# Kernel optimization log

Hardware: AMD Instinct MI355X
Metric: run time of the kernel (lower is better)

## Reference

```python
import math
import jax, jax.numpy as jnp
import numpy as np

B, N, C = 2, 2048, 256
TOPK_COARSE = 128
TOPK_FINE = 16
LOCAL_RAD = math.radians(15.0)
TEMP = 0.07
NEG = -1e9


def setup_inputs() -> dict:
    key = jax.random.key(0)
    ks = jax.random.split(key, 8)
    feat_a = jax.random.normal(ks[0], (B, N, C), jnp.float32)
    feat_b = jax.random.normal(ks[1], (B, N, C), jnp.float32)
    da = jax.random.normal(ks[2], (B, N, 3), jnp.float32)
    db = jax.random.normal(ks[3], (B, N, 3), jnp.float32)
    dirs_a = da / jnp.linalg.norm(da, axis=-1, keepdims=True)
    dirs_b = db / jnp.linalg.norm(db, axis=-1, keepdims=True)
    s = 1.0 / np.sqrt(C).astype(np.float32)
    Wq = jax.random.normal(ks[4], (C, C), jnp.float32) * s
    bq = jax.random.normal(ks[5], (C,), jnp.float32) * 0.01
    Wk = jax.random.normal(ks[6], (C, C), jnp.float32) * s
    bk = jax.random.normal(ks[7], (C,), jnp.float32) * 0.01
    return {"feat_a": feat_a, "feat_b": feat_b, "dirs_a": dirs_a, "dirs_b": dirs_b,
            "Wq": Wq, "bq": bq, "Wk": Wk, "bk": bk}


def reference(feat_a, feat_b, dirs_a, dirs_b, Wq, bq, Wk, bk):
    b, n, c = feat_a.shape
    q = feat_a @ Wq.T + bq                         # [B,N,C]
    k = feat_b @ Wk.T + bk                         # [B,N,C]

    # coarse stage: top-k over full similarity (math identical to chunked topk)
    sim = jnp.einsum('bnc,bmc->bnm', q, k)         # [B,N,N]
    _, coarse_idx = jax.lax.top_k(sim, TOPK_COARSE)  # [B,N,Kc]

    bi = jnp.arange(b)[:, None, None]
    k_cand = k[bi, coarse_idx]                     # [B,N,Kc,C]
    db_cand = dirs_b[bi, coarse_idx]               # [B,N,Kc,3]

    # angular locality mask (non-differentiable path)
    cosang = jnp.clip(jnp.sum(dirs_a[:, :, None, :] * db_cand, -1), -1.0, 1.0)
    ang = jnp.arccos(jax.lax.stop_gradient(cosang))
    local_mask = ang <= LOCAL_RAD                  # [B,N,Kc]
    # per-row fallback to all-ones (subsumes the chunk-level torch.any check)
    valid = local_mask.any(-1, keepdims=True)
    eff = jnp.where(valid, local_mask, True)

    logits_full = jnp.einsum('bnc,bnkc->bnk', q, k_cand) / TEMP
    logits_full = jnp.where(eff, logits_full, NEG)

    # fine stage: keep top TOPK_FINE candidates per row
    topk_vals, topk_pos = jax.lax.top_k(logits_full, TOPK_FINE)  # [B,N,Kf]
    idx = jnp.take_along_axis(coarse_idx, topk_pos, -1)
    eff_f = jnp.take_along_axis(eff, topk_pos, -1)
    fallback = eff_f.any(-1, keepdims=True)
    eff_f = jnp.where(fallback, eff_f, True)
    logits = jnp.where(eff_f, topk_vals, NEG)

    probs = jax.nn.softmax(logits, axis=-1) * eff_f.astype(logits.dtype)

    # scatter sparse support into dense P (indices distinct per row -> set is safe)
    ri = jnp.arange(n)[None, :, None]
    P = jnp.zeros((b, n, n), feat_a.dtype).at[bi, ri, idx].set(probs)
    P = P / (P.sum(-1, keepdims=True) + 1e-8)
    return P
```

## Files before the change

kernel.cpp:

```cpp
#include <hip/hip_runtime.h>
#include <hip/hip_bf16.h>
#include <math.h>

#define NN_ 2048
#define CC_ 256
#define KC_ 128
#define KF_ 16
#define EQCAP 64

typedef __attribute__((ext_vector_type(8))) short short8;
typedef __attribute__((ext_vector_type(4))) float f32x4;

__device__ __forceinline__ unsigned int mono_u(float f) {
  unsigned int u = __float_as_uint(f);
  return (u & 0x80000000u) ? ~u : (u | 0x80000000u);
}
__device__ __forceinline__ float inv_mono(unsigned int m) {
  unsigned int u = (m & 0x80000000u) ? (m ^ 0x80000000u) : ~m;
  return __uint_as_float(u);
}

__device__ __forceinline__ void gload_lds16(const void* g, void* l) {
  __builtin_amdgcn_global_load_lds(
      (const __attribute__((address_space(1))) void*)g,
      (__attribute__((address_space(3))) void*)l, 16, 0, 0);
}

__global__ __launch_bounds__(256) void proj_split_kernel(
    const float* __restrict__ fa, const float* __restrict__ fb,
    const float* __restrict__ Wq, const float* __restrict__ bq,
    const float* __restrict__ Wk, const float* __restrict__ bk,
    __hip_bfloat16* __restrict__ qh, __hip_bfloat16* __restrict__ ql,
    __hip_bfloat16* __restrict__ kh, __hip_bfloat16* __restrict__ kl)
{
  __shared__ float As2[32][32];
  __shared__ float Bs[32][64];
  const int z = blockIdx.z;
  const float* A = z ? fb : fa;
  const float* W = z ? Wk : Wq;
  const float* bias = z ? bk : bq;
  __hip_bfloat16* oh = z ? kh : qh;
  __hip_bfloat16* ol = z ? kl : ql;

  const int m0 = blockIdx.y * 32, n0 = blockIdx.x * 64;
  const int tid = threadIdx.x;
  const int tx = tid & 15, ty = tid >> 4;
  const int r = tid >> 3, c4 = (tid & 7) << 2;
  float acc[2][4] = {};
  for (int kb = 0; kb < CC_; kb += 32) {
    float4 va = *(const float4*)(A + (long)(m0 + r) * CC_ + kb + c4);
    As2[c4 + 0][r] = va.x; As2[c4 + 1][r] = va.y;
    As2[c4 + 2][r] = va.z; As2[c4 + 3][r] = va.w;
    float4 vb0 = *(const float4*)(W + (long)(n0 + r) * CC_ + kb + c4);
    Bs[c4 + 0][r] = vb0.x; Bs[c4 + 1][r] = vb0.y;
    Bs[c4 + 2][r] = vb0.z; Bs[c4 + 3][r] = vb0.w;
    float4 vb1 = *(const float4*)(W + (long)(n0 + r + 32) * CC_ + kb + c4);
    Bs[c4 + 0][r + 32] = vb1.x; Bs[c4 + 1][r + 32] = vb1.y;
    Bs[c4 + 2][r + 32] = vb1.z; Bs[c4 + 3][r + 32] = vb1.w;
    __syncthreads();
#pragma unroll
    for (int kk = 0; kk < 32; ++kk) {
      float a0 = As2[kk][(ty << 1)];
      float a1 = As2[kk][(ty << 1) + 1];
      float4 bv = *(const float4*)&Bs[kk][tx << 2];
      acc[0][0] += a0 * bv.x; acc[0][1] += a0 * bv.y;
      acc[0][2] += a0 * bv.z; acc[0][3] += a0 * bv.w;
      acc[1][0] += a1 * bv.x; acc[1][1] += a1 * bv.y;
      acc[1][2] += a1 * bv.z; acc[1][3] += a1 * bv.w;
    }
    __syncthreads();
  }
  float bv4[4];
#pragma unroll
  for (int j = 0; j < 4; ++j) bv4[j] = bias[n0 + (tx << 2) + j];
#pragma unroll
  for (int i = 0; i < 2; ++i) {
    int m = m0 + (ty << 1) + i;
    __hip_bfloat16 hv[4], lv[4];
#pragma unroll
    for (int j = 0; j < 4; ++j) {
      float v = acc[i][j] + bv4[j];
      __hip_bfloat16 h = __float2bfloat16(v);
      hv[j] = h;
      lv[j] = __float2bfloat16(v - __bfloat162float(h));
    }
    long base = (long)m * CC_ + n0 + (tx << 2);
    *(uint2*)(oh + base) = *(const uint2*)hv;
    *(uint2*)(ol + base) = *(const uint2*)lv;
  }
}

__global__ __launch_bounds__(256) void sim_mfma_kernel(
    const __hip_bfloat16* __restrict__ qh, const __hip_bfloat16* __restrict__ ql,
    const __hip_bfloat16* __restrict__ kh, const __hip_bfloat16* __restrict__ kl,
    float* __restrict__ sim)
{
  __shared__ short As[128 * 32];
  __shared__ short Bs[128 * 32];
  const int z = blockIdx.z;
  const long off = (long)z * NN_ * CC_;
  const __hip_bfloat16* Aseg[3] = {qh + off, qh + off, ql + off};
  const __hip_bfloat16* Bseg[3] = {kh + off, kl + off, kh + off};
  const int m0 = blockIdx.y * 128, n0 = blockIdx.x * 128;
  const int tid = threadIdx.x;
  const int lane = tid & 63, wave = tid >> 6;
  const int wm = (wave & 1) << 6, wn = (wave >> 1) << 6;
  const int fm = lane & 15, quad = lane >> 4;

  const int r0 = tid >> 2, r1 = r0 + 64;
  const int c0 = (((tid & 3) ^ ((r0 >> 1) & 3)) << 3);
  const int c1 = (((tid & 3) ^ ((r1 >> 1) & 3)) << 3);
  short* lA0 = As + (long)tid * 8;
  short* lA1 = As + ((long)tid + 256) * 8;
  short* lB0 = Bs + (long)tid * 8;
  short* lB1 = Bs + ((long)tid + 256) * 8;
  const long gA0 = (long)(m0 + r0) * CC_ + c0;
  const long gA1 = (long)(m0 + r1) * CC_ + c1;
  const long gB0 = (long)(n0 + r0) * CC_ + c0;
  const long gB1 = (long)(n0 + r1) * CC_ + c1;

  f32x4 acc[4][4];
#pragma unroll
  for (int i = 0; i < 4; ++i)
#pragma unroll
    for (int j = 0; j < 4; ++j)
      acc[i][j] = (f32x4){0.f, 0.f, 0.f, 0.f};

  for (int s = 0; s < 3; ++s) {
    const __hip_bfloat16* Ap = Aseg[s];
    const __hip_bfloat16* Bp = Bseg[s];
    for (int kb = 0; kb < CC_; kb += 32) {
      gload_lds16(Ap + gA0 + kb, lA0);
      gload_lds16(Ap + gA1 + kb, lA1);
      gload_lds16(Bp + gB0 + kb, lB0);
      gload_lds16(Bp + gB1 + kb, lB1);
      __syncthreads();
      short8 af[4], bf[4];
#pragma unroll
      for (int t = 0; t < 4; ++t) {
        int m = wm + (t << 4) + fm;
        af[t] = *(const short8*)&As[((m << 2) + (quad ^ ((m >> 1) & 3))) << 3];
        int n = wn + (t << 4) + fm;
        bf[t] = *(const short8*)&Bs[((n << 2) + (quad ^ ((n >> 1) & 3))) << 3];
      }
#pragma unroll
      for (int mi = 0; mi < 4; ++mi)
#pragma unroll
        for (int ni = 0; ni < 4; ++ni)
          acc[mi][ni] = __builtin_amdgcn_mfma_f32_16x16x32_bf16(
              af[mi], bf[ni], acc[mi][ni], 0, 0, 0);
      __syncthreads();
    }
  }

  float* Cp = sim + (long)z * NN_ * NN_;
#pragma unroll
  for (int mi = 0; mi < 4; ++mi) {
#pragma unroll
    for (int ni = 0; ni < 4; ++ni) {
      int m = m0 + wm + (mi << 4) + (quad << 2);
      int n = n0 + wn + (ni << 4) + fm;
      float* p = Cp + (long)m * NN_ + n;
      p[0] = acc[mi][ni][0];
      p[NN_] = acc[mi][ni][1];
      p[2 * NN_] = acc[mi][ni][2];
      p[3 * NN_] = acc[mi][ni][3];
    }
  }
}

__global__ __launch_bounds__(256) void select_scatter_kernel(
    const float* __restrict__ sim, const float* __restrict__ dirs_a,
    const float* __restrict__ dirs_b, float* __restrict__ P)
{
  const int wave = threadIdx.x >> 6;
  const int lane = threadIdx.x & 63;
  const int row = (blockIdx.x << 2) | wave;
  const int b = row >> 11;
  const float* srow = sim + (long)row * NN_;
  float* prow = P + (long)row * NN_;

  __shared__ unsigned int hist_s[4][256];
  __shared__ unsigned int ckey_s[4][KC_];
  __shared__ int cidx_s[4][KC_];
  __shared__ int eq_s[4][EQCAP];
  __shared__ float outp_s[4][KF_];
  __shared__ int outj_s[4][KF_];
  __shared__ float rowbuf_s[4][1024];
  __shared__ int cnt_s[4][2];

  unsigned int* hist = hist_s[wave];
  unsigned int* ckey = ckey_s[wave];
  int* cidx = cidx_s[wave];
  int* eqb = eq_s[wave];
  float* outp = outp_s[wave];
  int* outj = outj_s[wave];
  float* rowbuf = rowbuf_s[wave];
  int* cnt = cnt_s[wave];

  unsigned int key[32];
#pragma unroll
  for (int c = 0; c < 8; ++c) {
    float4 v = *(const float4*)(srow + (c << 8) + (lane << 2));
    key[(c << 2) + 0] = mono_u(v.x);
    key[(c << 2) + 1] = mono_u(v.y);
    key[(c << 2) + 2] = mono_u(v.z);
    key[(c << 2) + 3] = mono_u(v.w);
  }

  unsigned int prefix = 0u, pmask = 0u;
  int need = KC_;
  for (int pass = 0; pass < 4; ++pass) {
    const int sh = 24 - (pass << 3);
    uint4 z4; z4.x = z4.y = z4.z = z4.w = 0u;
    *(uint4*)&hist[lane << 2] = z4;
#pragma unroll
    for (int i = 0; i < 32; ++i) {
      unsigned int u = key[i];
      if ((u & pmask) == prefix) atomicAdd(&hist[(u >> sh) & 255u], 1u);
    }
    uint4 h = *(const uint4*)&hist[lane << 2];
    unsigned int s3 = h.w, s2 = h.z + s3, s1 = h.y + s2, s0 = h.x + s1;
    unsigned int tot = s0, incl = tot;
#pragma unroll
    for (int off = 1; off < 64; off <<= 1) {
      unsigned int y = __shfl_down(incl, off);
      incl += (lane + off < 64) ? y : 0u;
    }
    const unsigned int excl = incl - tot;
    unsigned int geq[4] = {s0 + excl, s1 + excl, s2 + excl, s3 + excl};
    unsigned int gt[4] = {s1 + excl, s2 + excl, s3 + excl, excl};
    int fbin = -1;
    unsigned int fgt = 0u;
#pragma unroll
    for (int i = 0; i < 4; ++i)
      if (fbin < 0 && geq[i] >= (unsigned)need && gt[i] < (unsigned)need) {
        fbin = (lane << 2) + i;
        fgt = gt[i];
      }
    unsigned long long mb = __ballot(fbin >= 0);
    int src = __ffsll(mb) - 1;
    int selbin = __shfl(fbin, src);
    unsigned int gtv = __shfl(fgt, src);
    prefix |= ((unsigned)(selbin & 255)) << sh;
    pmask |= 0xFFu << sh;
    need -= (int)gtv;
  }
  const unsigned int T = prefix;
  const int need_eq = need;
  const int count_gt = KC_ - need_eq;

  if (lane == 0) { cnt[0] = 0; cnt[1] = 0; }
#pragma unroll
  for (int i = 0; i < 32; ++i) {
    unsigned int u = key[i];
    int col = ((i >> 2) << 8) + (lane << 2) + (i & 3);
    if (u > T) {
      int p = atomicAdd(&cnt[0], 1);
      ckey[p] = u;
      cidx[p] = col;
    } else if (u == T) {
      int p = atomicAdd(&cnt[1], 1);
      if (p < EQCAP) eqb[p] = col;
    }
  }
  int neq = cnt[1];
  if (lane == 0) {
    if (neq <= EQCAP) {
      for (int r = 0; r < need_eq; ++r) {
        int best = 0x7FFFFFFF, bi = 0;
        for (int t2 = 0; t2 < neq; ++t2)
          if (eqb[t2] < best) { best = eqb[t2]; bi = t2; }
        eqb[bi] = 0x7FFFFFFF;
        ckey[count_gt + r] = T;
        cidx[count_gt + r] = best;
      }
    } else {
      int r2 = 0;
      for (int j = 0; j < NN_ && r2 < need_eq; ++j)
        if (mono_u(srow[j]) == T) {
          ckey[count_gt + r2] = T;
          cidx[count_gt + r2] = j;
          ++r2;
        }
    }
  }

  const long dbase = (long)row * 3;
  const float dax = dirs_a[dbase + 0], day = dirs_a[dbase + 1],
              daz = dirs_a[dbase + 2];
  int j0 = cidx[lane], j1 = cidx[lane + 64];
  float va0 = inv_mono(ckey[lane]), va1 = inv_mono(ckey[lane + 64]);
  const float* db0 = dirs_b + ((long)(b << 11) + j0) * 3;
  float ca0 = dax * db0[0] + day * db0[1] + daz * db0[2];
  const float* db1 = dirs_b + ((long)(b << 11) + j1) * 3;
  float ca1 = dax * db1[0] + day * db1[1] + daz * db1[2];
  bool lm0 = ca0 >= 0.96592582628906831f;
  bool lm1 = ca1 >= 0.96592582628906831f;
  int ecnt = __popcll(__ballot(lm0)) + __popcll(__ballot(lm1));
  const bool all = (ecnt == 0);
  float v0 = (all || lm0) ? va0 : -INFINITY;
  float v1 = (all || lm1) ? va1 : -INFINITY;
  const int elig = all ? KC_ : ecnt;
  const int nk = elig < KF_ ? elig : KF_;

  for (int r = 0; r < nk; ++r) {
    float bvv; int bj, bs;
    if (v1 > v0 || (v1 == v0 && j1 < j0)) { bvv = v1; bj = j1; bs = lane + 64; }
    else { bvv = v0; bj = j0; bs = lane; }
#pragma unroll
    for (int off = 32; off > 0; off >>= 1) {
      float ov = __shfl_down(bvv, off);
      int oj = __shfl_down(bj, off);
      int os = __shfl_down(bs, off);
      if (ov > bvv || (ov == bvv && oj < bj)) { bvv = ov; bj = oj; bs = os; }
    }
    bvv = __shfl(bvv, 0); bj = __shfl(bj, 0); bs = __shfl(bs, 0);
    if (lane == 0) { outj[r] = bj; outp[r] = bvv; }
    if (bs == lane) v0 = -INFINITY;
    if (bs == lane + 64) v1 = -INFINITY;
  }

  const float invT = 1.0f / 0.07f;
  float mxl = outp[0] * invT;
  float e = 0.f;
  int myj = 0;
  if (lane < nk) {
    e = __expf(outp[lane] * invT - mxl);
    myj = outj[lane];
  }
  float ssum = e;
#pragma unroll
  for (int off = 32; off > 0; off >>= 1) ssum += __shfl_xor(ssum, off);
  float pr = e / ssum;
  float s2 = pr;
#pragma unroll
  for (int off = 32; off > 0; off >>= 1) s2 += __shfl_xor(s2, off);
  const float outv = pr * (1.0f / (s2 + 1e-8f));

#pragma unroll
  for (int h = 0; h < 2; ++h) {
    float4 zf; zf.x = zf.y = zf.z = zf.w = 0.f;
#pragma unroll
    for (int q = 0; q < 4; ++q)
      *(float4*)&rowbuf[(q << 8) + (lane << 2)] = zf;
    if (lane < nk && (myj >> 10) == h) rowbuf[myj & 1023] = outv;
#pragma unroll
    for (int q = 0; q < 4; ++q) {
      float4 v = *(const float4*)&rowbuf[(q << 8) + (lane << 2)];
      *(float4*)(prow + (h << 10) + (q << 8) + (lane << 2)) = v;
    }
  }
}

extern "C" void kernel_launch(void* const* d_in, const int* in_sizes, int n_in,
                              void* d_out, int out_size, void* d_ws, size_t ws_size,
                              hipStream_t stream) {
  (void)in_sizes; (void)n_in; (void)out_size; (void)ws_size;
  const float* feat_a = (const float*)d_in[0];
  const float* feat_b = (const float*)d_in[1];
  const float* dirs_a = (const float*)d_in[2];
  const float* dirs_b = (const float*)d_in[3];
  const float* Wq = (const float*)d_in[4];
  const float* bq = (const float*)d_in[5];
  const float* Wk = (const float*)d_in[6];
  const float* bk = (const float*)d_in[7];
  float* P = (float*)d_out;

  __hip_bfloat16* qh = (__hip_bfloat16*)d_ws;
  __hip_bfloat16* ql = qh + (long)2 * NN_ * CC_;
  __hip_bfloat16* kh = ql + (long)2 * NN_ * CC_;
  __hip_bfloat16* kl = kh + (long)2 * NN_ * CC_;
  float* sim = (float*)(kl + (long)2 * NN_ * CC_);

  proj_split_kernel<<<dim3(CC_ / 64, (2 * NN_) / 32, 2), 256, 0, stream>>>(
      feat_a, feat_b, Wq, bq, Wk, bk, qh, ql, kh, kl);

  sim_mfma_kernel<<<dim3(NN_ / 128, NN_ / 128, 2), 256, 0, stream>>>(
      qh, ql, kh, kl, sim);

  select_scatter_kernel<<<dim3((2 * NN_) / 4), 256, 0, stream>>>(
      sim, dirs_a, dirs_b, P);
}
```

Baseline: 167.3 us.

## Use split-bf16 MFMA for projection and fuse sim passes into one K loop

The projection GEMM moves from scalar FP32 FMAs to MFMA, splitting inputs on the fly into high and low bf16 parts in LDS and issuing three MFMAs per tile. The similarity kernel loads the hi and lo halves of q and k together and does all three products in a single K sweep, replacing three separate sweeps that each reloaded tiles. This cuts global/LDS traffic and barriers at the cost of doubled LDS footprint, which may lower occupancy. The projection's precision changes slightly because its inputs are now split into bf16 pairs.

```diff
diff --git a/kernel.cpp b/kernel.cpp
--- a/kernel.cpp
+++ b/kernel.cpp
@@ -26,68 +26,144 @@
       (__attribute__((address_space(3))) void*)l, 16, 0, 0);
 }
 
-__global__ __launch_bounds__(256) void proj_split_kernel(
+__device__ __forceinline__ unsigned short bf16_bits(float v) {
+  __hip_bfloat16 h = __float2bfloat16(v);
+  return *(unsigned short*)&h;
+}
+__device__ __forceinline__ float bf16_val(unsigned short u) {
+  __hip_bfloat16 h = *(__hip_bfloat16*)&u;
+  return __bfloat162float(h);
+}
+
+__global__ __launch_bounds__(256) void proj_mfma_kernel(
     const float* __restrict__ fa, const float* __restrict__ fb,
     const float* __restrict__ Wq, const float* __restrict__ bq,
     const float* __restrict__ Wk, const float* __restrict__ bk,
     __hip_bfloat16* __restrict__ qh, __hip_bfloat16* __restrict__ ql,
     __hip_bfloat16* __restrict__ kh, __hip_bfloat16* __restrict__ kl)
 {
-  __shared__ float As2[32][32];
-  __shared__ float Bs[32][64];
-  const int z = blockIdx.z;
+  __shared__ short Ah[64 * 32], Al[64 * 32], Bh[64 * 32], Bl[64 * 32];
+  const int m0 = blockIdx.y * 64;
+  const int z = m0 >> 12;
+  const int mloc = m0 & 4095;
   const float* A = z ? fb : fa;
   const float* W = z ? Wk : Wq;
   const float* bias = z ? bk : bq;
   __hip_bfloat16* oh = z ? kh : qh;
   __hip_bfloat16* ol = z ? kl : ql;
-
-  const int m0 = blockIdx.y * 32, n0 = blockIdx.x * 64;
+  const int n0 = blockIdx.x * 64;
   const int tid = threadIdx.x;
-  const int tx = tid & 15, ty = tid >> 4;
-  const int r = tid >> 3, c4 = (tid & 7) << 2;
-  float acc[2][4] = {};
+  const int lane = tid & 63, wave = tid >> 6;
+  const int wm = (wave & 1) << 5, wn = (wave >> 1) << 5;
+  const int fm = lane & 15, quad = lane >> 4;
+
+  const int r = tid >> 3;
+  const int r2 = r + 32;
+  const int c4 = (tid & 7) << 2;
+  const int ck = c4 >> 3;
+  const int soff = c4 & 7;
+  const int iA0 = (((r << 2) + (ck ^ ((r >> 1) & 3))) << 3) + soff;
+  const int iA1 = (((r2 << 2) + (ck ^ ((r2 >> 1) & 3))) << 3) + soff;
+
+  f32x4 acc[2][2];
+#pragma unroll
+  for (int i = 0; i < 2; ++i)
+#pragma unroll
+    for (int j = 0; j < 2; ++j) acc[i][j] = (f32x4){0.f, 0.f, 0.f, 0.f};
+
   for (int kb = 0; kb < CC_; kb += 32) {
-    float4 va = *(const float4*)(A + (long)(m0 + r) * CC_ + kb + c4);
-    As2[c4 + 0][r] = va.x; As2[c4 + 1][r] = va.y;
-    As2[c4 + 2][r] = va.z; As2[c4 + 3][r] = va.w;
+    float4 va0 = *(const float4*)(A + (long)(mloc + r) * CC_ + kb + c4);
+    float4 va1 = *(const float4*)(A + (long)(mloc + r2) * CC_ + kb + c4);
     float4 vb0 = *(const float4*)(W + (long)(n0 + r) * CC_ + kb + c4);
-    Bs[c4 + 0][r] = vb0.x; Bs[c4 + 1][r] = vb0.y;
-    Bs[c4 + 2][r] = vb0.z; Bs[c4 + 3][r] = vb0.w;
-    float4 vb1 = *(const float4*)(W + (long)(n0 + r + 32) * CC_ + kb + c4);
-    Bs[c4 + 0][r + 32] = vb1.x; Bs[c4 + 1][r + 32] = vb1.y;
-    Bs[c4 + 2][r + 32] = vb1.z; Bs[c4 + 3][r + 32] = vb1.w;
+    float4 vb1 = *(const float4*)(W + (long)(n0 + r2) * CC_ + kb + c4);
     __syncthreads();
-#pragma unroll
-    for (int kk = 0; kk < 32; ++kk) {
-      float a0 = As2[kk][(ty << 1)];
-      float a1 = As2[kk][(ty << 1) + 1];
-      float4 bv = *(const float4*)&Bs[kk][tx << 2];
-      acc[0][0] += a0 * bv.x; acc[0][1] += a0 * bv.y;
-      acc[0][2] += a0 * bv.z; acc[0][3] += a0 * bv.w;
-      acc[1][0] += a1 * bv.x; acc[1][1] += a1 * bv.y;
-      acc[1][2] += a1 * bv.z; acc[1][3] += a1 * bv.w;
+    {
+      const float* pv;
+      float4 vv;
+      vv = va0; pv = (const float*)&vv;
+      uint2 hu, lu;
+      unsigned short h0 = bf16_bits(pv[0]), h1 = bf16_bits(pv[1]),
+                     h2 = bf16_bits(pv[2]), h3 = bf16_bits(pv[3]);
+      hu.x = (unsigned)h0 | ((unsigned)h1 << 16);
+      hu.y = (unsigned)h2 | ((unsigned)h3 << 16);
+      lu.x = (unsigned)bf16_bits(pv[0] - bf16_val(h0)) |
+             ((unsigned)bf16_bits(pv[1] - bf16_val(h1)) << 16);
+      lu.y = (unsigned)bf16_bits(pv[2] - bf16_val(h2)) |
+             ((unsigned)bf16_bits(pv[3] - bf16_val(h3)) << 16);
+      *(uint2*)&Ah[iA0] = hu; *(uint2*)&Al[iA0] = lu;
+      vv = va1; pv = (const float*)&vv;
+      h0 = bf16_bits(pv[0]); h1 = bf16_bits(pv[1]);
+      h2 = bf16_bits(pv[2]); h3 = bf16_bits(pv[3]);
+      hu.x = (unsigned)h0 | ((unsigned)h1 << 16);
+      hu.y = (unsigned)h2 | ((unsigned)h3 << 16);
+      lu.x = (unsigned)bf16_bits(pv[0] - bf16_val(h0)) |
+             ((unsigned)bf16_bits(pv[1] - bf16_val(h1)) << 16);
+      lu.y = (unsigned)bf16_bits(pv[2] - bf16_val(h2)) |
+             ((unsigned)bf16_bits(pv[3] - bf16_val(h3)) << 16);
+      *(uint2*)&Ah[iA1] = hu; *(uint2*)&Al[iA1] = lu;
+      vv = vb0; pv = (const float*)&vv;
+      h0 = bf16_bits(pv[0]); h1 = bf16_bits(pv[1]);
+      h2 = bf16_bits(pv[2]); h3 = bf16_bits(pv[3]);
+      hu.x = (unsigned)h0 | ((unsigned)h1 << 16);
+      hu.y = (unsigned)h2 | ((unsigned)h3 << 16);
+      lu.x = (unsigned)bf16_bits(pv[0] - bf16_val(h0)) |
+             ((unsigned)bf16_bits(pv[1] - bf16_val(h1)) << 16);
+      lu.y = (unsigned)bf16_bits(pv[2] - bf16_val(h2)) |
+             ((unsigned)bf16_bits(pv[3] - bf16_val(h3)) << 16);
+      *(uint2*)&Bh[iA0] = hu; *(uint2*)&Bl[iA0] = lu;
+      vv = vb1; pv = (const float*)&vv;
+      h0 = bf16_bits(pv[0]); h1 = bf16_bits(pv[1]);
+      h2 = bf16_bits(pv[2]); h3 = bf16_bits(pv[3]);
+      hu.x = (unsigned)h0 | ((unsigned)h1 << 16);
+      hu.y = (unsigned)h2 | ((unsigned)h3 << 16);
+      lu.x = (unsigned)bf16_bits(pv[0] - bf16_val(h0)) |
+             ((unsigned)bf16_bits(pv[1] - bf16_val(h1)) << 16);
+      lu.y = (unsigned)bf16_bits(pv[2] - bf16_val(h2)) |
+             ((unsigned)bf16_bits(pv[3] - bf16_val(h3)) << 16);
+      *(uint2*)&Bh[iA1] = hu; *(uint2*)&Bl[iA1] = lu;
     }
     __syncthreads();
-  }
-  float bv4[4];
-#pragma unroll
-  for (int j = 0; j < 4; ++j) bv4[j] = bias[n0 + (tx << 2) + j];
-#pragma unroll
-  for (int i = 0; i < 2; ++i) {
-    int m = m0 + (ty << 1) + i;
-    __hip_bfloat16 hv[4], lv[4];
-#pragma unroll
-    for (int j = 0; j < 4; ++j) {
-      float v = acc[i][j] + bv4[j];
-      __hip_bfloat16 h = __float2bfloat16(v);
-      hv[j] = h;
-      lv[j] = __float2bfloat16(v - __bfloat162float(h));
-    }
-    long base = (long)m * CC_ + n0 + (tx << 2);
-    *(uint2*)(oh + base) = *(const uint2*)hv;
-    *(uint2*)(ol + base) = *(const uint2*)lv;
-  }
+    short8 afh[2], afl[2], bfh[2], bfl[2];
+#pragma unroll
+    for (int t = 0; t < 2; ++t) {
+      int m = wm + (t << 4) + fm;
+      int sa = ((m << 2) + (quad ^ ((m >> 1) & 3))) << 3;
+      afh[t] = *(const short8*)&Ah[sa];
+      afl[t] = *(const short8*)&Al[sa];
+      int n = wn + (t << 4) + fm;
+      int sb = ((n << 2) + (quad ^ ((n >> 1) & 3))) << 3;
+      bfh[t] = *(const short8*)&Bh[sb];
+      bfl[t] = *(const short8*)&Bl[sb];
+    }
+#pragma unroll
+    for (int mi = 0; mi < 2; ++mi)
+#pragma unroll
+      for (int ni = 0; ni < 2; ++ni) {
+        acc[mi][ni] = __builtin_amdgcn_mfma_f32_16x16x32_bf16(
+            afh[mi], bfh[ni], acc[mi][ni], 0, 0, 0);
+        acc[mi][ni] = __builtin_amdgcn_mfma_f32_16x16x32_bf16(
+            afh[mi], bfl[ni], acc[mi][ni], 0, 0, 0);
+        acc[mi][ni] = __builtin_amdgcn_mfma_f32_16x16x32_bf16(
+            afl[mi], bfh[ni], acc[mi][ni], 0, 0, 0);
+      }
+  }
+
+#pragma unroll
+  for (int mi = 0; mi < 2; ++mi)
+#pragma unroll
+    for (int ni = 0; ni < 2; ++ni) {
+      int nn = n0 + wn + (ni << 4) + fm;
+      float bval = bias[nn];
+      int mrow = mloc + wm + (mi << 4) + (quad << 2);
+#pragma unroll
+      for (int reg = 0; reg < 4; ++reg) {
+        float v = acc[mi][ni][reg] + bval;
+        __hip_bfloat16 h = __float2bfloat16(v);
+        long idx = (long)(mrow + reg) * CC_ + nn;
+        oh[idx] = h;
+        ol[idx] = __float2bfloat16(v - __bfloat162float(h));
+      }
+    }
 }
 
 __global__ __launch_bounds__(256) void sim_mfma_kernel(
@@ -95,12 +171,9 @@
     const __hip_bfloat16* __restrict__ kh, const __hip_bfloat16* __restrict__ kl,
     float* __restrict__ sim)
 {
-  __shared__ short As[128 * 32];
-  __shared__ short Bs[128 * 32];
+  __shared__ short Ah[128 * 32], Al[128 * 32], Bh[128 * 32], Bl[128 * 32];
   const int z = blockIdx.z;
   const long off = (long)z * NN_ * CC_;
-  const __hip_bfloat16* Aseg[3] = {qh + off, qh + off, ql + off};
-  const __hip_bfloat16* Bseg[3] = {kh + off, kl + off, kh + off};
   const int m0 = blockIdx.y * 128, n0 = blockIdx.x * 128;
   const int tid = threadIdx.x;
   const int lane = tid & 63, wave = tid >> 6;
@@ -110,47 +183,52 @@
   const int r0 = tid >> 2, r1 = r0 + 64;
   const int c0 = (((tid & 3) ^ ((r0 >> 1) & 3)) << 3);
   const int c1 = (((tid & 3) ^ ((r1 >> 1) & 3)) << 3);
-  short* lA0 = As + (long)tid * 8;
-  short* lA1 = As + ((long)tid + 256) * 8;
-  short* lB0 = Bs + (long)tid * 8;
-  short* lB1 = Bs + ((long)tid + 256) * 8;
-  const long gA0 = (long)(m0 + r0) * CC_ + c0;
-  const long gA1 = (long)(m0 + r1) * CC_ + c1;
-  const long gB0 = (long)(n0 + r0) * CC_ + c0;
-  const long gB1 = (long)(n0 + r1) * CC_ + c1;
+  const long lo0 = (long)tid * 8, lo1 = ((long)tid + 256) * 8;
+  const long gA0 = (long)(m0 + r0) * CC_ + c0 + off;
+  const long gA1 = (long)(m0 + r1) * CC_ + c1 + off;
+  const long gB0 = (long)(n0 + r0) * CC_ + c0 + off;
+  const long gB1 = (long)(n0 + r1) * CC_ + c1 + off;
 
   f32x4 acc[4][4];
 #pragma unroll
   for (int i = 0; i < 4; ++i)
 #pragma unroll
-    for (int j = 0; j < 4; ++j)
-      acc[i][j] = (f32x4){0.f, 0.f, 0.f, 0.f};
-
-  for (int s = 0; s < 3; ++s) {
-    const __hip_bfloat16* Ap = Aseg[s];
-    const __hip_bfloat16* Bp = Bseg[s];
-    for (int kb = 0; kb < CC_; kb += 32) {
-      gload_lds16(Ap + gA0 + kb, lA0);
-      gload_lds16(Ap + gA1 + kb, lA1);
-      gload_lds16(Bp + gB0 + kb, lB0);
-      gload_lds16(Bp + gB1 + kb, lB1);
-      __syncthreads();
-      short8 af[4], bf[4];
-#pragma unroll
-      for (int t = 0; t < 4; ++t) {
-        int m = wm + (t << 4) + fm;
-        af[t] = *(const short8*)&As[((m << 2) + (quad ^ ((m >> 1) & 3))) << 3];
-        int n = wn + (t << 4) + fm;
-        bf[t] = *(const short8*)&Bs[((n << 2) + (quad ^ ((n >> 1) & 3))) << 3];
+    for (int j = 0; j < 4; ++j) acc[i][j] = (f32x4){0.f, 0.f, 0.f, 0.f};
+
+  for (int kb = 0; kb < CC_; kb += 32) {
+    gload_lds16(qh + gA0 + kb, Ah + lo0);
+    gload_lds16(qh + gA1 + kb, Ah + lo1);
+    gload_lds16(ql + gA0 + kb, Al + lo0);
+    gload_lds16(ql + gA1 + kb, Al + lo1);
+    gload_lds16(kh + gB0 + kb, Bh + lo0);
+    gload_lds16(kh + gB1 + kb, Bh + lo1);
+    gload_lds16(kl + gB0 + kb, Bl + lo0);
+    gload_lds16(kl + gB1 + kb, Bl + lo1);
+    __syncthreads();
+    short8 afh[4], afl[4], bfh[4], bfl[4];
+#pragma unroll
+    for (int t = 0; t < 4; ++t) {
+      int m = wm + (t << 4) + fm;
+      int sa = ((m << 2) + (quad ^ ((m >> 1) & 3))) << 3;
+      afh[t] = *(const short8*)&Ah[sa];
+      afl[t] = *(const short8*)&Al[sa];
+      int n = wn + (t << 4) + fm;
+      int sb = ((n << 2) + (quad ^ ((n >> 1) & 3))) << 3;
+      bfh[t] = *(const short8*)&Bh[sb];
+      bfl[t] = *(const short8*)&Bl[sb];
+    }
+#pragma unroll
+    for (int mi = 0; mi < 4; ++mi)
+#pragma unroll
+      for (int ni = 0; ni < 4; ++ni) {
+        acc[mi][ni] = __builtin_amdgcn_mfma_f32_16x16x32_bf16(
+            afh[mi], bfh[ni], acc[mi][ni], 0, 0, 0);
+        acc[mi][ni] = __builtin_amdgcn_mfma_f32_16x16x32_bf16(
+            afh[mi], bfl[ni], acc[mi][ni], 0, 0, 0);
+        acc[mi][ni] = __builtin_amdgcn_mfma_f32_16x16x32_bf16(
+            afl[mi], bfh[ni], acc[mi][ni], 0, 0, 0);
       }
-#pragma unroll
-      for (int mi = 0; mi < 4; ++mi)
-#pragma unroll
-        for (int ni = 0; ni < 4; ++ni)
-          acc[mi][ni] = __builtin_amdgcn_mfma_f32_16x16x32_bf16(
-              af[mi], bf[ni], acc[mi][ni], 0, 0, 0);
-      __syncthreads();
-    }
+    __syncthreads();
   }
 
   float* Cp = sim + (long)z * NN_ * NN_;
@@ -373,7 +451,7 @@
   __hip_bfloat16* kl = kh + (long)2 * NN_ * CC_;
   float* sim = (float*)(kl + (long)2 * NN_ * CC_);
 
-  proj_split_kernel<<<dim3(CC_ / 64, (2 * NN_) / 32, 2), 256, 0, stream>>>(
+  proj_mfma_kernel<<<dim3(CC_ / 64, (4 * NN_) / 64), 256, 0, stream>>>(
       feat_a, feat_b, Wq, bq, Wk, bk, qh, ql, kh, kl);
 
   sim_mfma_kernel<<<dim3(NN_ / 128, NN_ / 128, 2), 256, 0, stream>>>(
```

Result: faster. 143.3 us (-14.3%).
